# Performance work log

Measured on AMD Instinct MI355X. Metric: run time of the kernel, lower is better.

The kernel has to match this reference:

```python
import jax, jax.numpy as jnp
import numpy as np

FEAT = 256
HID = FEAT // 2
N_KEYS = 2          # output_keys = ["energy_0", "energy_1"]
N_MOLS = 2000
ATOMS_PER_MOL = 100
N_ATOMS = N_MOLS * ATOMS_PER_MOL
LOG2 = 0.6931471805599453


def shifted_softplus(x):
    # NFF's shifted softplus: softplus(x) - log(2)
    return jax.nn.softplus(x) - LOG2


def setup_inputs() -> dict:
    key = jax.random.key(0)
    ks = jax.random.split(key, 6)
    s_i = jax.random.normal(ks[0], (N_ATOMS, FEAT), dtype=jnp.float32)
    xyz = jax.random.normal(ks[1], (N_ATOMS, 3), dtype=jnp.float32)
    num_atoms = jnp.full((N_MOLS,), ATOMS_PER_MOL, dtype=jnp.int64)
    # Per-key MLP params stacked over keys: Linear(F->H), act, Linear(H->1)
    W1 = jax.random.normal(ks[2], (N_KEYS, FEAT, HID), dtype=jnp.float32) / np.sqrt(FEAT)
    b1 = jnp.zeros((N_KEYS, HID), dtype=jnp.float32)
    W2 = jax.random.normal(ks[3], (N_KEYS, HID), dtype=jnp.float32) / np.sqrt(HID)
    b2 = jnp.zeros((N_KEYS,), dtype=jnp.float32)
    return {"s_i": s_i, "xyz": xyz, "num_atoms": num_atoms,
            "W1": W1, "b1": b1, "W2": W2, "b2": b2}


def reference(s_i, xyz, num_atoms, W1, b1, W2, b2):
    n_mols = num_atoms.shape[0]
    # segment id per atom, replacing the torch.split(...)+per-chunk sum loop
    seg = jnp.repeat(jnp.arange(n_mols), num_atoms,
                     total_repeat_length=s_i.shape[0])        # [N]
    # per-key MLP: [K,N,H] hidden, [K,N] scalar output per atom
    h = shifted_softplus(jnp.einsum('nf,kfh->knh', s_i, W1) + b1[:, None, :])
    val = jnp.einsum('knh,kh->kn', h, W2) + b2[:, None]       # [K, N]
    # fused segment-sum pooling -> per-molecule scalars
    pooled = jax.ops.segment_sum(val.T, seg, num_segments=n_mols)  # [M, K]
    return pooled.T                                            # [K, M]
```

## Files before the change

kernel.cpp:

```cpp
#include <hip/hip_runtime.h>

#define FEAT 256
#define HID 128
#define NKEYS 2

typedef __bf16 bf16x8 __attribute__((ext_vector_type(8)));
typedef float f32x16 __attribute__((ext_vector_type(16)));

union Frag {
    bf16x8 v;
    unsigned u[4];
    uint4 q;
};

__device__ __forceinline__ void load_lds16(const float* g, void* l) {
    __builtin_amdgcn_global_load_lds(
        (const __attribute__((address_space(1))) unsigned int*)g,
        (__attribute__((address_space(3))) unsigned int*)l,
        16, 0, 0);
}

__device__ __forceinline__ unsigned pack_bf16_u2(unsigned u0, unsigned u1) {
    u0 += 0x8000u;
    u1 += 0x8000u;
    return __builtin_amdgcn_perm(u1, u0, 0x07060302u);
}

__device__ __forceinline__ float ssp(float x) {
    float sp = __logf(1.0f + __expf(x));
    sp = (x > 15.0f) ? x : sp;
    return sp - 0.69314718056f;
}

__device__ __forceinline__ int find_mol(const int* __restrict__ off, int n_mols, int g) {
    int lo = 0, hi = n_mols;
    while (hi - lo > 1) {
        int mid = (lo + hi) >> 1;
        if (off[mid] <= g) lo = mid; else hi = mid;
    }
    return lo;
}

__global__ void prep_kernel(const void* __restrict__ num_atoms_raw,
                            const float* __restrict__ W1,
                            int n_mols, int n_atoms,
                            int* __restrict__ off,
                            unsigned short* __restrict__ Bp,
                            float* __restrict__ out, int out_n) {
    if (blockIdx.x > 0) {
        int idx = (blockIdx.x - 1) * 256 + threadIdx.x;
        int c = idx >> 8;
        int k = idx & 255;
        int key = c >> 7, j = c & 127;
        float f = W1[(size_t)key * FEAT * HID + (size_t)k * HID + j];
        unsigned u = __float_as_uint(f);
        unsigned r = (u + 0x7FFFu + ((u >> 16) & 1u)) >> 16;
        Bp[(size_t)c * FEAT + k] = (unsigned short)r;
        return;
    }
    for (int i = threadIdx.x; i < out_n; i += 256) out[i] = 0.0f;

    __shared__ long long tsum[256];
    __shared__ int csum[257];
    __shared__ int mode_sh;
    int tid = threadIdx.x;
    const int* a32 = (const int*)num_atoms_raw;
    const long long* a64 = (const long long*)num_atoms_raw;
    int chunk = (n_mols + 255) >> 8;
    int lo = tid * chunk;
    if (lo > n_mols) lo = n_mols;
    int hi = lo + chunk;
    if (hi > n_mols) hi = n_mols;
    long long s = 0;
    for (int i = lo; i < hi; ++i) s += (long long)a32[i];
    tsum[tid] = s;
    __syncthreads();
    if (tid == 0) {
        long long t = 0;
        for (int i = 0; i < 256; ++i) t += tsum[i];
        mode_sh = (t == (long long)n_atoms) ? 0 : 1;
    }
    __syncthreads();
    int mode = mode_sh;
    if (mode) {
        s = 0;
        for (int i = lo; i < hi; ++i) s += a64[i];
        tsum[tid] = s;
    }
    csum[tid] = (int)tsum[tid];
    __syncthreads();
    if (tid == 0) {
        int run = 0;
        for (int i = 0; i < 256; ++i) { int v = csum[i]; csum[i] = run; run += v; }
    }
    __syncthreads();
    int run = csum[tid];
    for (int i = lo; i < hi; ++i) {
        off[i] = run;
        run += mode ? (int)a64[i] : a32[i];
    }
    if (hi >= n_mols) off[n_mols] = run;
}

__global__ __launch_bounds__(256, 2)
void gemm_fused(const float* __restrict__ A,
                const unsigned short* __restrict__ Bp,
                const float* __restrict__ b1,
                const float* __restrict__ W2,
                const float* __restrict__ b2,
                const int* __restrict__ off,
                float* __restrict__ out,
                int n_atoms, int n_mols) {
    __shared__ uint4 ldsA[64 * 64];
    __shared__ float part[4][64];
    __shared__ float molacc[NKEYS][4];

    const int tid  = threadIdx.x;
    const int lane = tid & 63;
    const int wn   = tid >> 6;
    const int l31  = lane & 31;
    const int half = lane >> 5;
    const int m0   = blockIdx.x * 64;

    #pragma unroll
    for (int i = 0; i < 16; ++i) {
        const int r = wn * 16 + i;
        int grow = m0 + r;
        if (grow > n_atoms - 1) grow = n_atoms - 1;
        const float* gp = A + (size_t)grow * FEAT + (((lane - r) & 63) << 2);
        load_lds16(gp, (void*)&ldsA[r * 64]);
    }

    const int c0 = wn * 64 + l31;
    const unsigned short* bb0 = Bp + (size_t)c0 * FEAT + half * 8;
    const unsigned short* bb1 = Bp + (size_t)(c0 + 32) * FEAT + half * 8;
    Frag bf0[2][4], bf1[2][4];
    #pragma unroll
    for (int s = 0; s < 2; ++s)
        #pragma unroll
        for (int j = 0; j < 4; ++j) {
            bf0[s][j].q = *(const uint4*)(bb0 + s * 64 + j * 16);
            bf1[s][j].q = *(const uint4*)(bb1 + s * 64 + j * 16);
        }

    __syncthreads();

    const int rb0 = l31 * 64;
    const int rb1 = (l31 + 32) * 64;

    f32x16 acc00 = 0.0f, acc01 = 0.0f, acc10 = 0.0f, acc11 = 0.0f;

    #pragma unroll
    for (int c = 0; c < 4; ++c) {
        const int slot = c & 1;
        #pragma unroll
        for (int j = 0; j < 4; ++j) {
            const int g0 = c * 16 + j * 4 + half * 2;
            uint4 q0 = ldsA[rb0 + ((g0     + l31) & 63)];
            uint4 q1 = ldsA[rb0 + ((g0 + 1 + l31) & 63)];
            uint4 r0 = ldsA[rb1 + ((g0     + l31 + 32) & 63)];
            uint4 r1 = ldsA[rb1 + ((g0 + 1 + l31 + 32) & 63)];
            Frag a0, a1;
            a0.u[0] = pack_bf16_u2(q0.x, q0.y);
            a0.u[1] = pack_bf16_u2(q0.z, q0.w);
            a0.u[2] = pack_bf16_u2(q1.x, q1.y);
            a0.u[3] = pack_bf16_u2(q1.z, q1.w);
            a1.u[0] = pack_bf16_u2(r0.x, r0.y);
            a1.u[1] = pack_bf16_u2(r0.z, r0.w);
            a1.u[2] = pack_bf16_u2(r1.x, r1.y);
            a1.u[3] = pack_bf16_u2(r1.z, r1.w);
            acc00 = __builtin_amdgcn_mfma_f32_32x32x16_bf16(a0.v, bf0[slot][j].v, acc00, 0, 0, 0);
            acc01 = __builtin_amdgcn_mfma_f32_32x32x16_bf16(a0.v, bf1[slot][j].v, acc01, 0, 0, 0);
            acc10 = __builtin_amdgcn_mfma_f32_32x32x16_bf16(a1.v, bf0[slot][j].v, acc10, 0, 0, 0);
            acc11 = __builtin_amdgcn_mfma_f32_32x32x16_bf16(a1.v, bf1[slot][j].v, acc11, 0, 0, 0);
        }
        if (c + 2 < 4) {
            const int kb = (c + 2) * 64;
            #pragma unroll
            for (int j = 0; j < 4; ++j) {
                bf0[slot][j].q = *(const uint4*)(bb0 + kb + j * 16);
                bf1[slot][j].q = *(const uint4*)(bb1 + kb + j * 16);
            }
        }
    }

    if (tid < NKEYS * 4) molacc[tid >> 2][tid & 3] = 0.0f;

    float b1c0 = b1[c0], b1c1 = b1[c0 + 32];
    float w2c0 = W2[c0], w2c1 = W2[c0 + 32];

    #pragma unroll
    for (int rt = 0; rt < 2; ++rt) {
        const f32x16& Ac0 = rt ? acc10 : acc00;
        const f32x16& Ac1 = rt ? acc11 : acc01;
        #pragma unroll
        for (int r = 0; r < 16; ++r) {
            float t = ssp(Ac0[r] + b1c0) * w2c0 + ssp(Ac1[r] + b1c1) * w2c1;
            t += __shfl_xor(t, 1);
            t += __shfl_xor(t, 2);
            t += __shfl_xor(t, 4);
            t += __shfl_xor(t, 8);
            t += __shfl_xor(t, 16);
            if (l31 == r) {
                int row = rt * 32 + (r & 3) + 8 * (r >> 2) + 4 * half;
                part[wn][row] = t;
            }
        }
    }
    __syncthreads();

    if (tid < NKEYS * 64) {
        int key = tid >> 6, r = tid & 63;
        int gm = m0 + r;
        if (gm < n_atoms) {
            float val = part[2 * key][r] + part[2 * key + 1][r] + b2[key];
            int mol  = find_mol(off, n_mols, gm);
            int mol0 = find_mol(off, n_mols, m0);
            int ml = mol - mol0;
            if (ml < 4) atomicAdd(&molacc[key][ml], val);
            else        atomicAdd(&out[(size_t)key * n_mols + mol], val);
        }
    }
    __syncthreads();

    if (tid < NKEYS * 4) {
        int key = tid >> 2, ml = tid & 3;
        int mol0 = find_mol(off, n_mols, m0);
        int mol = mol0 + ml;
        if (mol < n_mols) {
            float v = molacc[key][ml];
            if (v != 0.0f) atomicAdd(&out[(size_t)key * n_mols + mol], v);
        }
    }
}

extern "C" void kernel_launch(void* const* d_in, const int* in_sizes, int n_in,
                              void* d_out, int out_size, void* d_ws, size_t ws_size,
                              hipStream_t stream) {
    const float* s_i      = (const float*)d_in[0];
    const void*  num_atoms = d_in[2];
    const float* W1 = (const float*)d_in[3];
    const float* b1 = (const float*)d_in[4];
    const float* W2 = (const float*)d_in[5];
    const float* b2 = (const float*)d_in[6];
    int n_atoms = in_sizes[0] / FEAT;
    int n_mols  = in_sizes[2];
    float* out = (float*)d_out;

    int* off = (int*)d_ws;
    size_t off_bytes = (((size_t)(n_mols + 1) * 4) + 255) & ~(size_t)255;
    unsigned short* Bp = (unsigned short*)((char*)d_ws + off_bytes);

    int pack_blocks = (NKEYS * HID * FEAT) / 256;
    prep_kernel<<<1 + pack_blocks, 256, 0, stream>>>(num_atoms, W1, n_mols, n_atoms,
                                                     off, Bp, out, out_size);

    int gblocks = (n_atoms + 63) / 64;
    gemm_fused<<<gblocks, 256, 0, stream>>>(s_i, Bp, b1, W2, b2, off, out, n_atoms, n_mols);
}
```

Measured before the change: 375.4 us.

## Pre-swizzle W1 into fragment order and pad LDS rows instead of rotated global_load_lds

The prep kernel now writes bf16 W1 in the exact per-lane MFMA fragment order, so each B fragment load is a fully coalesced uint4 per lane. The A tile staging replaces direct global-to-LDS loads with a rotated address by register loads followed by LDS stores into rows padded to 1040 bytes, which avoids bank conflicts without the rotation arithmetic. The register staging adds VGPR pressure (16 uint4 per thread) and removes the asynchronous global_load_lds path, so load latency may now be less hidden.

```diff
diff --git a/kernel.cpp b/kernel.cpp
--- a/kernel.cpp
+++ b/kernel.cpp
@@ -6,6 +6,8 @@
 
 typedef __bf16 bf16x8 __attribute__((ext_vector_type(8)));
 typedef float f32x16 __attribute__((ext_vector_type(16)));
+
+#define LDS_ROW 1040
 
 union Frag {
     bf16x8 v;
@@ -13,13 +15,6 @@
     uint4 q;
 };
 
-__device__ __forceinline__ void load_lds16(const float* g, void* l) {
-    __builtin_amdgcn_global_load_lds(
-        (const __attribute__((address_space(1))) unsigned int*)g,
-        (__attribute__((address_space(3))) unsigned int*)l,
-        16, 0, 0);
-}
-
 __device__ __forceinline__ unsigned pack_bf16_u2(unsigned u0, unsigned u1) {
     u0 += 0x8000u;
     u1 += 0x8000u;
@@ -45,17 +40,25 @@
                             const float* __restrict__ W1,
                             int n_mols, int n_atoms,
                             int* __restrict__ off,
-                            unsigned short* __restrict__ Bp,
+                            unsigned short* __restrict__ Bp2,
                             float* __restrict__ out, int out_n) {
     if (blockIdx.x > 0) {
         int idx = (blockIdx.x - 1) * 256 + threadIdx.x;
-        int c = idx >> 8;
-        int k = idx & 255;
-        int key = c >> 7, j = c & 127;
-        float f = W1[(size_t)key * FEAT * HID + (size_t)k * HID + j];
+        int arr  = (idx >> 15) & 1;
+        int w    = (idx >> 13) & 3;
+        int c    = (idx >> 11) & 3;
+        int jj   = (idx >> 9)  & 3;
+        int lane = (idx >> 3)  & 63;
+        int e    = idx & 7;
+        int l31 = lane & 31, half = lane >> 5;
+        int row = w * 64 + l31 + arr * 32;
+        int k   = c * 64 + jj * 16 + half * 8 + e;
+        int key = row >> 7, jh = row & 127;
+        float f = W1[(size_t)key * FEAT * HID + (size_t)k * HID + jh];
         unsigned u = __float_as_uint(f);
         unsigned r = (u + 0x7FFFu + ((u >> 16) & 1u)) >> 16;
-        Bp[(size_t)c * FEAT + k] = (unsigned short)r;
+        size_t out_idx = ((size_t)(arr * 4096 + ((w * 4 + c) * 4 + jj) * 64 + lane)) * 8 + e;
+        Bp2[out_idx] = (unsigned short)r;
         return;
     }
     for (int i = threadIdx.x; i < out_n; i += 256) out[i] = 0.0f;
@@ -104,14 +107,14 @@
 
 __global__ __launch_bounds__(256, 2)
 void gemm_fused(const float* __restrict__ A,
-                const unsigned short* __restrict__ Bp,
+                const uint4* __restrict__ Bp2,
                 const float* __restrict__ b1,
                 const float* __restrict__ W2,
                 const float* __restrict__ b2,
                 const int* __restrict__ off,
                 float* __restrict__ out,
                 int n_atoms, int n_mols) {
-    __shared__ uint4 ldsA[64 * 64];
+    __shared__ unsigned char ldsAraw[64 * LDS_ROW];
     __shared__ float part[4][64];
     __shared__ float molacc[NKEYS][4];
 
@@ -122,31 +125,37 @@
     const int half = lane >> 5;
     const int m0   = blockIdx.x * 64;
 
-    #pragma unroll
-    for (int i = 0; i < 16; ++i) {
-        const int r = wn * 16 + i;
-        int grow = m0 + r;
-        if (grow > n_atoms - 1) grow = n_atoms - 1;
-        const float* gp = A + (size_t)grow * FEAT + (((lane - r) & 63) << 2);
-        load_lds16(gp, (void*)&ldsA[r * 64]);
-    }
-
-    const int c0 = wn * 64 + l31;
-    const unsigned short* bb0 = Bp + (size_t)c0 * FEAT + half * 8;
-    const unsigned short* bb1 = Bp + (size_t)(c0 + 32) * FEAT + half * 8;
+    {
+        uint4 q[16];
+        #pragma unroll
+        for (int i = 0; i < 16; ++i) {
+            const int r = wn * 16 + i;
+            int grow = m0 + r;
+            if (grow > n_atoms - 1) grow = n_atoms - 1;
+            q[i] = *(const uint4*)(A + (size_t)grow * FEAT + lane * 4);
+        }
+        #pragma unroll
+        for (int i = 0; i < 16; ++i) {
+            const int r = wn * 16 + i;
+            *(uint4*)(ldsAraw + r * LDS_ROW + lane * 16) = q[i];
+        }
+    }
+
+    const uint4* B0 = Bp2;
+    const uint4* B1 = Bp2 + 4096;
     Frag bf0[2][4], bf1[2][4];
     #pragma unroll
     for (int s = 0; s < 2; ++s)
         #pragma unroll
         for (int j = 0; j < 4; ++j) {
-            bf0[s][j].q = *(const uint4*)(bb0 + s * 64 + j * 16);
-            bf1[s][j].q = *(const uint4*)(bb1 + s * 64 + j * 16);
-        }
-
-    __syncthreads();
-
-    const int rb0 = l31 * 64;
-    const int rb1 = (l31 + 32) * 64;
+            bf0[s][j].q = B0[(((wn * 4) + s) * 4 + j) * 64 + lane];
+            bf1[s][j].q = B1[(((wn * 4) + s) * 4 + j) * 64 + lane];
+        }
+
+    __syncthreads();
+
+    const unsigned char* rbp0 = ldsAraw + l31 * LDS_ROW;
+    const unsigned char* rbp1 = ldsAraw + (l31 + 32) * LDS_ROW;
 
     f32x16 acc00 = 0.0f, acc01 = 0.0f, acc10 = 0.0f, acc11 = 0.0f;
 
@@ -155,11 +164,11 @@
         const int slot = c & 1;
         #pragma unroll
         for (int j = 0; j < 4; ++j) {
-            const int g0 = c * 16 + j * 4 + half * 2;
-            uint4 q0 = ldsA[rb0 + ((g0     + l31) & 63)];
-            uint4 q1 = ldsA[rb0 + ((g0 + 1 + l31) & 63)];
-            uint4 r0 = ldsA[rb1 + ((g0     + l31 + 32) & 63)];
-            uint4 r1 = ldsA[rb1 + ((g0 + 1 + l31 + 32) & 63)];
+            const int g0 = (c * 16 + j * 4 + half * 2) * 16;
+            uint4 q0 = *(const uint4*)(rbp0 + g0);
+            uint4 q1 = *(const uint4*)(rbp0 + g0 + 16);
+            uint4 r0 = *(const uint4*)(rbp1 + g0);
+            uint4 r1 = *(const uint4*)(rbp1 + g0 + 16);
             Frag a0, a1;
             a0.u[0] = pack_bf16_u2(q0.x, q0.y);
             a0.u[1] = pack_bf16_u2(q0.z, q0.w);
@@ -175,17 +184,17 @@
             acc11 = __builtin_amdgcn_mfma_f32_32x32x16_bf16(a1.v, bf1[slot][j].v, acc11, 0, 0, 0);
         }
         if (c + 2 < 4) {
-            const int kb = (c + 2) * 64;
             #pragma unroll
             for (int j = 0; j < 4; ++j) {
-                bf0[slot][j].q = *(const uint4*)(bb0 + kb + j * 16);
-                bf1[slot][j].q = *(const uint4*)(bb1 + kb + j * 16);
+                bf0[slot][j].q = B0[(((wn * 4) + (c + 2)) * 4 + j) * 64 + lane];
+                bf1[slot][j].q = B1[(((wn * 4) + (c + 2)) * 4 + j) * 64 + lane];
             }
         }
     }
 
     if (tid < NKEYS * 4) molacc[tid >> 2][tid & 3] = 0.0f;
 
+    const int c0 = wn * 64 + l31;
     float b1c0 = b1[c0], b1c1 = b1[c0 + 32];
     float w2c0 = W2[c0], w2c1 = W2[c0 + 32];
 
@@ -249,12 +258,13 @@
 
     int* off = (int*)d_ws;
     size_t off_bytes = (((size_t)(n_mols + 1) * 4) + 255) & ~(size_t)255;
-    unsigned short* Bp = (unsigned short*)((char*)d_ws + off_bytes);
+    unsigned short* Bp2 = (unsigned short*)((char*)d_ws + off_bytes);
 
     int pack_blocks = (NKEYS * HID * FEAT) / 256;
     prep_kernel<<<1 + pack_blocks, 256, 0, stream>>>(num_atoms, W1, n_mols, n_atoms,
-                                                     off, Bp, out, out_size);
+                                                     off, Bp2, out, out_size);
 
     int gblocks = (n_atoms + 63) / 64;
-    gemm_fused<<<gblocks, 256, 0, stream>>>(s_i, Bp, b1, W2, b2, off, out, n_atoms, n_mols);
-}
+    gemm_fused<<<gblocks, 256, 0, stream>>>(s_i, (const uint4*)Bp2, b1, W2, b2, off,
+                                            out, n_atoms, n_mols);
+}
```

Measured after the change: 388.2 us. 1.03x slower.
